# Kernel tuning notes

Measured on AMD Instinct MI355X. Metric: run time of the kernel, lower is better.

The kernel has to match this reference:

```python
import jax, jax.numpy as jnp
import numpy as np

H = 128          # hidden_dim
N = 64           # max_nodes == nodes per graph
G = 512          # num_graphs
E = N * (N - 1) // 2  # policy slots per graph (2016)
LN_EPS = 1e-5


def setup_inputs() -> dict:
    key = jax.random.key(0)
    ks = jax.random.split(key, 8)
    # Complete undirected graph per batch element: canonical edges (i<j), contiguous node blocks.
    iu, ju = np.triu_indices(N, k=1)                      # each [E]
    offs = np.arange(G)[:, None] * N                      # [G,1]
    src = (offs + iu[None, :]).reshape(-1)                # [G*E]
    dst = (offs + ju[None, :]).reshape(-1)
    edge_index = jnp.asarray(np.stack([src, dst]), dtype=jnp.int32)   # [2, G*E]
    num_edges = G * E
    edge_features = jax.random.normal(ks[0], (num_edges, H), dtype=jnp.float32)
    batch = jnp.repeat(jnp.arange(G, dtype=jnp.int32), N)             # [G*N]
    num_nodes_per_graph = jnp.full((G,), N, dtype=jnp.int32)
    s = 0.02
    return {
        "edge_features": edge_features,
        "edge_index": edge_index,
        "batch": batch,
        "num_nodes_per_graph": num_nodes_per_graph,
        "ln_g": jnp.ones((H,), jnp.float32),
        "ln_b": jnp.zeros((H,), jnp.float32),
        "W1": jax.random.normal(ks[1], (H, H), jnp.float32) * s,
        "b1": jnp.zeros((H,), jnp.float32),
        "W2": jax.random.normal(ks[2], (H, H // 2), jnp.float32) * s,
        "b2": jnp.zeros((H // 2,), jnp.float32),
        "W3": jax.random.normal(ks[3], (H // 2, 1), jnp.float32) * s,
        "b3": jnp.zeros((1,), jnp.float32),
    }


def _policy_net(x, ln_g, ln_b, W1, b1, W2, b2, W3, b3):
    mu = jnp.mean(x, axis=-1, keepdims=True)
    var = jnp.mean(jnp.square(x - mu), axis=-1, keepdims=True)
    x = (x - mu) * jax.lax.rsqrt(var + LN_EPS) * ln_g + ln_b
    x = jax.nn.gelu(x @ W1 + b1, approximate=False)   # torch nn.GELU default = exact erf
    x = jax.nn.gelu(x @ W2 + b2, approximate=False)   # (dropout is identity in eval)
    return (x @ W3 + b3)[:, 0]                        # [num_edges]


def reference(edge_features, edge_index, batch, num_nodes_per_graph,
              ln_g, ln_b, W1, b1, W2, b2, W3, b3):
    scores = _policy_net(edge_features, ln_g, ln_b, W1, b1, W2, b2, W3, b3)
    src, dst = edge_index[0], edge_index[1]
    g = src // N                                       # graph id (contiguous node blocks of N)
    ls, ld = src - g * N, dst - g * N                  # local node ids
    i = jnp.minimum(ls, ld)
    j = jnp.maximum(ls, ld)
    # canonical upper-triangular index: i*N - i(i+1)/2 + (j-i-1)
    idx = i * N - i * (i + 1) // 2 + (j - i - 1)
    flat = g * E + idx                                 # [num_edges]
    valid = ls != ld
    logits = jnp.zeros((G * E,), scores.dtype).at[jnp.where(valid, flat, G * E)].set(
        scores, mode="drop")
    return jax.nn.softmax(logits.reshape(G, E), axis=-1)
```

## Files before the change

kernel.cpp:

```cpp
#include <hip/hip_runtime.h>
#include <math.h>

constexpr int Hdim  = 128;
constexpr int Npn   = 64;
constexpr int Eg    = 2016;
constexpr int Gg    = 512;
constexpr int TOT   = Gg * Eg;
constexpr int PITCH = 136;

typedef unsigned short ushortx8 __attribute__((ext_vector_type(8)));
typedef __bf16         bf16x8   __attribute__((ext_vector_type(8)));
typedef float          floatx4  __attribute__((ext_vector_type(4)));

static __device__ __forceinline__ unsigned short f2bf(float f) {
    unsigned int u = __float_as_uint(f);
    u += 0x7FFFu + ((u >> 16) & 1u);
    return (unsigned short)(u >> 16);
}

static __device__ __forceinline__ float gelu_exact(float x) {
    return 0.5f * x * (1.0f + erff(x * 0.70710678118654752440f));
}

static __device__ __forceinline__ floatx4 mfma16(ushortx8 a, ushortx8 b, floatx4 c) {
    return __builtin_amdgcn_mfma_f32_16x16x32_bf16(
        __builtin_bit_cast(bf16x8, a), __builtin_bit_cast(bf16x8, b), c, 0, 0, 0);
}

__global__ __launch_bounds__(256, 3)
void scores_kernel(const float* __restrict__ X, const int* __restrict__ ei,
                   const float* __restrict__ lng, const float* __restrict__ lnb,
                   const float* __restrict__ W1, const float* __restrict__ b1,
                   const float* __restrict__ W2, const float* __restrict__ b2,
                   const float* __restrict__ W3, const float* __restrict__ b3,
                   float* __restrict__ out)
{
    __shared__ unsigned short Xl[64 * PITCH];
    __shared__ unsigned short H1l[64 * PITCH];
    __shared__ float part[4 * 64];

    const int tid  = threadIdx.x;
    const int wave = tid >> 6;
    const int lane = tid & 63;
    const int q    = lane >> 4;
    const int c16  = lane & 15;

    ushortx8 B1f[2][4];
#pragma unroll
    for (int c = 0; c < 2; ++c) {
        const int n = (2 * wave + c) * 16 + c16;
#pragma unroll
        for (int kt = 0; kt < 4; ++kt) {
            ushortx8 f;
#pragma unroll
            for (int j = 0; j < 8; ++j)
                f[j] = f2bf(W1[(kt * 32 + q * 8 + j) * Hdim + n]);
            B1f[c][kt] = f;
        }
    }
    const int n2 = wave * 16 + c16;
    ushortx8 B2f[4];
#pragma unroll
    for (int kt = 0; kt < 4; ++kt) {
        ushortx8 f;
#pragma unroll
        for (int j = 0; j < 8; ++j)
            f[j] = f2bf(W2[(kt * 32 + q * 8 + j) * 64 + n2]);
        B2f[kt] = f;
    }

    const float b1v0 = b1[(2 * wave) * 16 + c16];
    const float b1v1 = b1[(2 * wave + 1) * 16 + c16];
    const float b2v  = b2[n2];
    const float w3v  = W3[n2];
    const float b3v  = b3[0];

    const float4 g4  = ((const float4*)lng)[tid & 31];
    const float4 bb4 = ((const float4*)lnb)[tid & 31];

    for (int t = 0; t < 4; ++t) {
        const int row0 = (blockIdx.x * 4 + t) * 64;

        const float4* Xg = (const float4*)X + (size_t)row0 * 32;
#pragma unroll
        for (int i = 0; i < 8; ++i) {
            float4 v = Xg[tid + 256 * i];
            float s  = v.x + v.y + v.z + v.w;
            float s2 = v.x * v.x + v.y * v.y + v.z * v.z + v.w * v.w;
#pragma unroll
            for (int m = 1; m < 32; m <<= 1) {
                s  += __shfl_xor(s, m);
                s2 += __shfl_xor(s2, m);
            }
            const float mu  = s * 0.0078125f;
            const float var = s2 * 0.0078125f - mu * mu;
            const float rs  = rsqrtf(var + 1e-5f);
            const int row   = (tid + 256 * i) >> 5;
            const float y0 = (v.x - mu) * rs * g4.x + bb4.x;
            const float y1 = (v.y - mu) * rs * g4.y + bb4.y;
            const float y2 = (v.z - mu) * rs * g4.z + bb4.z;
            const float y3 = (v.w - mu) * rs * g4.w + bb4.w;
            uint2 pk;
            pk.x = (unsigned)f2bf(y0) | ((unsigned)f2bf(y1) << 16);
            pk.y = (unsigned)f2bf(y2) | ((unsigned)f2bf(y3) << 16);
            *reinterpret_cast<uint2*>(&Xl[row * PITCH + (tid & 31) * 4]) = pk;
        }
        __syncthreads();

        floatx4 acc[4][2];
#pragma unroll
        for (int rt = 0; rt < 4; ++rt)
#pragma unroll
            for (int c = 0; c < 2; ++c)
                acc[rt][c] = floatx4{0.f, 0.f, 0.f, 0.f};

#pragma unroll
        for (int kt = 0; kt < 4; ++kt) {
            ushortx8 a[4];
#pragma unroll
            for (int rt = 0; rt < 4; ++rt)
                a[rt] = *reinterpret_cast<const ushortx8*>(
                    &Xl[(rt * 16 + c16) * PITCH + kt * 32 + q * 8]);
#pragma unroll
            for (int rt = 0; rt < 4; ++rt) {
                acc[rt][0] = mfma16(a[rt], B1f[0][kt], acc[rt][0]);
                acc[rt][1] = mfma16(a[rt], B1f[1][kt], acc[rt][1]);
            }
        }

#pragma unroll
        for (int rt = 0; rt < 4; ++rt) {
#pragma unroll
            for (int c = 0; c < 2; ++c) {
                const float bb = c ? b1v1 : b1v0;
                const int col  = (2 * wave + c) * 16 + c16;
#pragma unroll
                for (int r = 0; r < 4; ++r) {
                    const float h = gelu_exact(acc[rt][c][r] + bb);
                    H1l[(rt * 16 + q * 4 + r) * PITCH + col] = f2bf(h);
                }
            }
        }
        __syncthreads();

        floatx4 acc2[4];
#pragma unroll
        for (int rt = 0; rt < 4; ++rt) acc2[rt] = floatx4{0.f, 0.f, 0.f, 0.f};
#pragma unroll
        for (int kt = 0; kt < 4; ++kt) {
            ushortx8 a[4];
#pragma unroll
            for (int rt = 0; rt < 4; ++rt)
                a[rt] = *reinterpret_cast<const ushortx8*>(
                    &H1l[(rt * 16 + c16) * PITCH + kt * 32 + q * 8]);
#pragma unroll
            for (int rt = 0; rt < 4; ++rt)
                acc2[rt] = mfma16(a[rt], B2f[kt], acc2[rt]);
        }

#pragma unroll
        for (int rt = 0; rt < 4; ++rt) {
            floatx4 pv;
#pragma unroll
            for (int r = 0; r < 4; ++r)
                pv[r] = gelu_exact(acc2[rt][r] + b2v) * w3v;
#pragma unroll
            for (int m = 1; m < 16; m <<= 1) {
#pragma unroll
                for (int r = 0; r < 4; ++r) pv[r] += __shfl_xor(pv[r], m);
            }
            if (c16 == 0)
                *reinterpret_cast<floatx4*>(&part[wave * 64 + rt * 16 + q * 4]) = pv;
        }
        __syncthreads();

        if (tid < 64) {
            const float sc = b3v + part[tid] + part[64 + tid] + part[128 + tid] + part[192 + tid];
            const int e  = row0 + tid;
            const int s  = ei[e];
            const int d  = ei[TOT + e];
            const int g  = s >> 6;
            const int ls = s & 63, ld = d & 63;
            const int i2 = min(ls, ld), j2 = max(ls, ld);
            if (ls != ld) {
                const int idx = i2 * Npn - ((i2 * (i2 + 1)) >> 1) + (j2 - i2 - 1);
                out[g * Eg + idx] = sc;
            }
        }
        __syncthreads();
    }
}

__global__ __launch_bounds__(256)
void softmax_kernel(float* __restrict__ buf)
{
    __shared__ float red[4];
    const int tid  = threadIdx.x;
    const int wave = tid >> 6;
    const int lane = tid & 63;
    const int base = blockIdx.x * Eg;

    float v[8];
    float mx = -3.4e38f;
#pragma unroll
    for (int k = 0; k < 8; ++k) {
        const int idx = tid + 256 * k;
        v[k] = (idx < Eg) ? buf[base + idx] : -3.4e38f;
        mx = fmaxf(mx, v[k]);
    }
#pragma unroll
    for (int m = 1; m < 64; m <<= 1) mx = fmaxf(mx, __shfl_xor(mx, m));
    if (lane == 0) red[wave] = mx;
    __syncthreads();
    mx = fmaxf(fmaxf(red[0], red[1]), fmaxf(red[2], red[3]));
    __syncthreads();

    float sum = 0.f;
#pragma unroll
    for (int k = 0; k < 8; ++k) {
        const int idx = tid + 256 * k;
        if (idx < Eg) {
            v[k] = expf(v[k] - mx);
            sum += v[k];
        }
    }
#pragma unroll
    for (int m = 1; m < 64; m <<= 1) sum += __shfl_xor(sum, m);
    if (lane == 0) red[wave] = sum;
    __syncthreads();
    sum = red[0] + red[1] + red[2] + red[3];
    const float inv = 1.0f / sum;

#pragma unroll
    for (int k = 0; k < 8; ++k) {
        const int idx = tid + 256 * k;
        if (idx < Eg) buf[base + idx] = v[k] * inv;
    }
}

extern "C" void kernel_launch(void* const* d_in, const int* in_sizes, int n_in,
                              void* d_out, int out_size, void* d_ws, size_t ws_size,
                              hipStream_t stream)
{
    const float* Xf  = (const float*)d_in[0];
    const int*   ei  = (const int*)d_in[1];
    const float* lng = (const float*)d_in[4];
    const float* lnb = (const float*)d_in[5];
    const float* W1  = (const float*)d_in[6];
    const float* b1  = (const float*)d_in[7];
    const float* W2  = (const float*)d_in[8];
    const float* b2  = (const float*)d_in[9];
    const float* W3  = (const float*)d_in[10];
    const float* b3  = (const float*)d_in[11];
    float* out = (float*)d_out;

    hipLaunchKernelGGL(scores_kernel, dim3(TOT / 256), dim3(256), 0, stream,
                       Xf, ei, lng, lnb, W1, b1, W2, b2, W3, b3, out);
    hipLaunchKernelGGL(softmax_kernel, dim3(Gg), dim3(256), 0, stream, out);
}
```

Measured before the change: 786.1 us.

## Prefetch X tiles into LDS asynchronously, fold LayerNorm affine into W1, use fast GELU

```diff
diff --git a/kernel.cpp b/kernel.cpp
--- a/kernel.cpp
+++ b/kernel.cpp
@@ -6,6 +6,9 @@
 constexpr int Eg    = 2016;
 constexpr int Gg    = 512;
 constexpr int TOT   = Gg * Eg;
+constexpr int ROWS  = 32;
+constexpr int TPB   = 16;
+constexpr int NBLK  = TOT / (ROWS * TPB);
 constexpr int PITCH = 136;
 
 typedef unsigned short ushortx8 __attribute__((ext_vector_type(8)));
@@ -18,8 +21,23 @@
     return (unsigned short)(u >> 16);
 }
 
-static __device__ __forceinline__ float gelu_exact(float x) {
-    return 0.5f * x * (1.0f + erff(x * 0.70710678118654752440f));
+static __device__ __forceinline__ unsigned int cvt_pk_bf16(float lo, float hi) {
+    unsigned int r;
+    asm("v_cvt_pk_bf16_f32 %0, %1, %2" : "=v"(r) : "v"(lo), "v"(hi));
+    return r;
+}
+
+static __device__ __forceinline__ float gelu_fast(float x) {
+    const float z = fabsf(x) * 0.70710678118654752440f;
+    const float t = __builtin_amdgcn_rcpf(fmaf(0.3275911f, z, 1.0f));
+    float p = fmaf(1.061405429f, t, -1.453152027f);
+    p = fmaf(p, t,  1.421413741f);
+    p = fmaf(p, t, -0.284496736f);
+    p = fmaf(p, t,  0.254829592f);
+    p *= t;
+    const float e  = __builtin_amdgcn_exp2f(z * z * -1.4426950408889634f);
+    const float er = fmaf(-p, e, 1.0f);
+    return 0.5f * x * (1.0f + copysignf(er, x));
 }
 
 static __device__ __forceinline__ floatx4 mfma16(ushortx8 a, ushortx8 b, floatx4 c) {
@@ -27,7 +45,14 @@
         __builtin_bit_cast(bf16x8, a), __builtin_bit_cast(bf16x8, b), c, 0, 0, 0);
 }
 
-__global__ __launch_bounds__(256, 3)
+typedef __attribute__((address_space(1))) const unsigned int gu32;
+typedef __attribute__((address_space(3))) unsigned int       lu32;
+
+static __device__ __forceinline__ void gload_lds16(const float* g, float* l) {
+    __builtin_amdgcn_global_load_lds((gu32*)(const void*)g, (lu32*)(void*)l, 16, 0, 0);
+}
+
+__global__ __launch_bounds__(256, 4)
 void scores_kernel(const float* __restrict__ X, const int* __restrict__ ei,
                    const float* __restrict__ lng, const float* __restrict__ lnb,
                    const float* __restrict__ W1, const float* __restrict__ b1,
@@ -35,9 +60,10 @@
                    const float* __restrict__ W3, const float* __restrict__ b3,
                    float* __restrict__ out)
 {
-    __shared__ unsigned short Xl[64 * PITCH];
-    __shared__ unsigned short H1l[64 * PITCH];
-    __shared__ float part[4 * 64];
+    __shared__ float          raw[ROWS * Hdim];
+    __shared__ unsigned short Xl [ROWS * PITCH];
+    __shared__ unsigned short H1l[ROWS * PITCH];
+    __shared__ float          part[4 * ROWS];
 
     const int tid  = threadIdx.x;
     const int wave = tid >> 6;
@@ -45,18 +71,37 @@
     const int q    = lane >> 4;
     const int c16  = lane & 15;
 
+    const size_t blockRow0 = (size_t)blockIdx.x * (ROWS * TPB);
+
+    {
+        const float* src = X + blockRow0 * Hdim;
+        const int fo = wave * 256 + lane * 4;
+#pragma unroll
+        for (int k = 0; k < 4; ++k)
+            gload_lds16(src + fo + k * 1024, raw + wave * 256 + k * 1024);
+    }
+
     ushortx8 B1f[2][4];
+    float    b1v[2];
 #pragma unroll
     for (int c = 0; c < 2; ++c) {
         const int n = (2 * wave + c) * 16 + c16;
+        float pb = 0.f;
 #pragma unroll
         for (int kt = 0; kt < 4; ++kt) {
             ushortx8 f;
 #pragma unroll
-            for (int j = 0; j < 8; ++j)
-                f[j] = f2bf(W1[(kt * 32 + q * 8 + j) * Hdim + n]);
+            for (int j = 0; j < 8; ++j) {
+                const int k = kt * 32 + q * 8 + j;
+                const float w = W1[k * Hdim + n];
+                pb   = fmaf(lnb[k], w, pb);
+                f[j] = f2bf(lng[k] * w);
+            }
             B1f[c][kt] = f;
         }
+        pb += __shfl_xor(pb, 16);
+        pb += __shfl_xor(pb, 32);
+        b1v[c] = b1[n] + pb;
     }
     const int n2 = wave * 16 + c16;
     ushortx8 B2f[4];
@@ -68,126 +113,130 @@
             f[j] = f2bf(W2[(kt * 32 + q * 8 + j) * 64 + n2]);
         B2f[kt] = f;
     }
-
-    const float b1v0 = b1[(2 * wave) * 16 + c16];
-    const float b1v1 = b1[(2 * wave + 1) * 16 + c16];
-    const float b2v  = b2[n2];
-    const float w3v  = W3[n2];
-    const float b3v  = b3[0];
-
-    const float4 g4  = ((const float4*)lng)[tid & 31];
-    const float4 bb4 = ((const float4*)lnb)[tid & 31];
-
-    for (int t = 0; t < 4; ++t) {
-        const int row0 = (blockIdx.x * 4 + t) * 64;
-
-        const float4* Xg = (const float4*)X + (size_t)row0 * 32;
-#pragma unroll
-        for (int i = 0; i < 8; ++i) {
-            float4 v = Xg[tid + 256 * i];
-            float s  = v.x + v.y + v.z + v.w;
-            float s2 = v.x * v.x + v.y * v.y + v.z * v.z + v.w * v.w;
-#pragma unroll
-            for (int m = 1; m < 32; m <<= 1) {
-                s  += __shfl_xor(s, m);
-                s2 += __shfl_xor(s2, m);
-            }
-            const float mu  = s * 0.0078125f;
-            const float var = s2 * 0.0078125f - mu * mu;
-            const float rs  = rsqrtf(var + 1e-5f);
-            const int row   = (tid + 256 * i) >> 5;
-            const float y0 = (v.x - mu) * rs * g4.x + bb4.x;
-            const float y1 = (v.y - mu) * rs * g4.y + bb4.y;
-            const float y2 = (v.z - mu) * rs * g4.z + bb4.z;
-            const float y3 = (v.w - mu) * rs * g4.w + bb4.w;
+    const float b2v = b2[n2];
+    const float w3v = W3[n2];
+    const float b3v = b3[0];
+
+    const int row = tid >> 3;
+    const int cg  = tid & 7;
+
+    __syncthreads();
+
+    for (int t = 0; t < TPB; ++t) {
+        float4 x[4];
+#pragma unroll
+        for (int k = 0; k < 4; ++k)
+            x[k] = *reinterpret_cast<const float4*>(&raw[row * Hdim + cg * 4 + k * 32]);
+        float s = 0.f, s2 = 0.f;
+#pragma unroll
+        for (int k = 0; k < 4; ++k) {
+            s += x[k].x + x[k].y + x[k].z + x[k].w;
+            s2 = fmaf(x[k].x, x[k].x, s2);
+            s2 = fmaf(x[k].y, x[k].y, s2);
+            s2 = fmaf(x[k].z, x[k].z, s2);
+            s2 = fmaf(x[k].w, x[k].w, s2);
+        }
+        s  += __shfl_xor(s, 1);  s  += __shfl_xor(s, 2);  s  += __shfl_xor(s, 4);
+        s2 += __shfl_xor(s2, 1); s2 += __shfl_xor(s2, 2); s2 += __shfl_xor(s2, 4);
+        const float mu  = s * 0.0078125f;
+        const float var = fmaf(s2, 0.0078125f, -mu * mu);
+        const float rs  = rsqrtf(var + 1e-5f);
+        const float nm  = -mu * rs;
+#pragma unroll
+        for (int k = 0; k < 4; ++k) {
             uint2 pk;
-            pk.x = (unsigned)f2bf(y0) | ((unsigned)f2bf(y1) << 16);
-            pk.y = (unsigned)f2bf(y2) | ((unsigned)f2bf(y3) << 16);
-            *reinterpret_cast<uint2*>(&Xl[row * PITCH + (tid & 31) * 4]) = pk;
+            pk.x = cvt_pk_bf16(fmaf(x[k].x, rs, nm), fmaf(x[k].y, rs, nm));
+            pk.y = cvt_pk_bf16(fmaf(x[k].z, rs, nm), fmaf(x[k].w, rs, nm));
+            *reinterpret_cast<uint2*>(&Xl[row * PITCH + cg * 4 + k * 32]) = pk;
         }
         __syncthreads();
 
-        floatx4 acc[4][2];
-#pragma unroll
-        for (int rt = 0; rt < 4; ++rt)
+        if (t + 1 < TPB) {
+            const float* src = X + (blockRow0 + (size_t)(t + 1) * ROWS) * Hdim;
+            const int fo = wave * 256 + lane * 4;
+#pragma unroll
+            for (int k = 0; k < 4; ++k)
+                gload_lds16(src + fo + k * 1024, raw + wave * 256 + k * 1024);
+        }
+        int sv = 0, dv = 0;
+        const int e = (int)(blockRow0 + (size_t)t * ROWS) + tid;
+        if (tid < ROWS) { sv = ei[e]; dv = ei[TOT + e]; }
+
+        floatx4 acc[2][2];
+#pragma unroll
+        for (int rt = 0; rt < 2; ++rt)
 #pragma unroll
             for (int c = 0; c < 2; ++c)
                 acc[rt][c] = floatx4{0.f, 0.f, 0.f, 0.f};
-
 #pragma unroll
         for (int kt = 0; kt < 4; ++kt) {
-            ushortx8 a[4];
-#pragma unroll
-            for (int rt = 0; rt < 4; ++rt)
-                a[rt] = *reinterpret_cast<const ushortx8*>(
-                    &Xl[(rt * 16 + c16) * PITCH + kt * 32 + q * 8]);
-#pragma unroll
-            for (int rt = 0; rt < 4; ++rt) {
-                acc[rt][0] = mfma16(a[rt], B1f[0][kt], acc[rt][0]);
-                acc[rt][1] = mfma16(a[rt], B1f[1][kt], acc[rt][1]);
+            ushortx8 a0 = *reinterpret_cast<const ushortx8*>(&Xl[(c16)      * PITCH + kt * 32 + q * 8]);
+            ushortx8 a1 = *reinterpret_cast<const ushortx8*>(&Xl[(16 + c16) * PITCH + kt * 32 + q * 8]);
+            acc[0][0] = mfma16(a0, B1f[0][kt], acc[0][0]);
+            acc[0][1] = mfma16(a0, B1f[1][kt], acc[0][1]);
+            acc[1][0] = mfma16(a1, B1f[0][kt], acc[1][0]);
+            acc[1][1] = mfma16(a1, B1f[1][kt], acc[1][1]);
+        }
+
+#pragma unroll
+        for (int rt = 0; rt < 2; ++rt) {
+#pragma unroll
+            for (int c = 0; c < 2; ++c) {
+                const float bb = b1v[c];
+                const int col  = (2 * wave + c) * 16 + c16;
+                const float h0 = gelu_fast(acc[rt][c][0] + bb);
+                const float h1 = gelu_fast(acc[rt][c][1] + bb);
+                const float h2 = gelu_fast(acc[rt][c][2] + bb);
+                const float h3 = gelu_fast(acc[rt][c][3] + bb);
+                const unsigned int p01 = cvt_pk_bf16(h0, h1);
+                const unsigned int p23 = cvt_pk_bf16(h2, h3);
+                const int rbase = rt * 16 + q * 4;
+                H1l[(rbase + 0) * PITCH + col] = (unsigned short)p01;
+                H1l[(rbase + 1) * PITCH + col] = (unsigned short)(p01 >> 16);
+                H1l[(rbase + 2) * PITCH + col] = (unsigned short)p23;
+                H1l[(rbase + 3) * PITCH + col] = (unsigned short)(p23 >> 16);
             }
         }
-
-#pragma unroll
-        for (int rt = 0; rt < 4; ++rt) {
-#pragma unroll
-            for (int c = 0; c < 2; ++c) {
-                const float bb = c ? b1v1 : b1v0;
-                const int col  = (2 * wave + c) * 16 + c16;
-#pragma unroll
-                for (int r = 0; r < 4; ++r) {
-                    const float h = gelu_exact(acc[rt][c][r] + bb);
-                    H1l[(rt * 16 + q * 4 + r) * PITCH + col] = f2bf(h);
-                }
-            }
-        }
         __syncthreads();
 
-        floatx4 acc2[4];
-#pragma unroll
-        for (int rt = 0; rt < 4; ++rt) acc2[rt] = floatx4{0.f, 0.f, 0.f, 0.f};
+        floatx4 acc2[2];
+        acc2[0] = floatx4{0.f, 0.f, 0.f, 0.f};
+        acc2[1] = floatx4{0.f, 0.f, 0.f, 0.f};
 #pragma unroll
         for (int kt = 0; kt < 4; ++kt) {
-            ushortx8 a[4];
-#pragma unroll
-            for (int rt = 0; rt < 4; ++rt)
-                a[rt] = *reinterpret_cast<const ushortx8*>(
-                    &H1l[(rt * 16 + c16) * PITCH + kt * 32 + q * 8]);
-#pragma unroll
-            for (int rt = 0; rt < 4; ++rt)
-                acc2[rt] = mfma16(a[rt], B2f[kt], acc2[rt]);
-        }
-
-#pragma unroll
-        for (int rt = 0; rt < 4; ++rt) {
+            ushortx8 a0 = *reinterpret_cast<const ushortx8*>(&H1l[(c16)      * PITCH + kt * 32 + q * 8]);
+            ushortx8 a1 = *reinterpret_cast<const ushortx8*>(&H1l[(16 + c16) * PITCH + kt * 32 + q * 8]);
+            acc2[0] = mfma16(a0, B2f[kt], acc2[0]);
+            acc2[1] = mfma16(a1, B2f[kt], acc2[1]);
+        }
+
+#pragma unroll
+        for (int rt = 0; rt < 2; ++rt) {
             floatx4 pv;
 #pragma unroll
             for (int r = 0; r < 4; ++r)
-                pv[r] = gelu_exact(acc2[rt][r] + b2v) * w3v;
+                pv[r] = gelu_fast(acc2[rt][r] + b2v) * w3v;
 #pragma unroll
             for (int m = 1; m < 16; m <<= 1) {
 #pragma unroll
                 for (int r = 0; r < 4; ++r) pv[r] += __shfl_xor(pv[r], m);
             }
             if (c16 == 0)
-                *reinterpret_cast<floatx4*>(&part[wave * 64 + rt * 16 + q * 4]) = pv;
+                *reinterpret_cast<floatx4*>(&part[wave * ROWS + rt * 16 + q * 4]) = pv;
         }
         __syncthreads();
 
-        if (tid < 64) {
-            const float sc = b3v + part[tid] + part[64 + tid] + part[128 + tid] + part[192 + tid];
-            const int e  = row0 + tid;
-            const int s  = ei[e];
-            const int d  = ei[TOT + e];
-            const int g  = s >> 6;
-            const int ls = s & 63, ld = d & 63;
+        if (tid < ROWS) {
+            const float sc = b3v + part[tid] + part[ROWS + tid]
+                           + part[2 * ROWS + tid] + part[3 * ROWS + tid];
+            const int g  = sv >> 6;
+            const int ls = sv & 63, ld = dv & 63;
             const int i2 = min(ls, ld), j2 = max(ls, ld);
             if (ls != ld) {
                 const int idx = i2 * Npn - ((i2 * (i2 + 1)) >> 1) + (j2 - i2 - 1);
                 out[g * Eg + idx] = sc;
             }
         }
-        __syncthreads();
     }
 }
 
@@ -220,7 +269,7 @@
     for (int k = 0; k < 8; ++k) {
         const int idx = tid + 256 * k;
         if (idx < Eg) {
-            v[k] = expf(v[k] - mx);
+            v[k] = __builtin_amdgcn_exp2f((v[k] - mx) * 1.4426950408889634f);
             sum += v[k];
         }
     }
@@ -254,7 +303,7 @@
     const float* b3  = (const float*)d_in[11];
     float* out = (float*)d_out;
 
-    hipLaunchKernelGGL(scores_kernel, dim3(TOT / 256), dim3(256), 0, stream,
+    hipLaunchKernelGGL(scores_kernel, dim3(NBLK), dim3(256), 0, stream,
                        Xf, ei, lng, lnb, W1, b1, W2, b2, W3, b3, out);
     hipLaunchKernelGGL(softmax_kernel, dim3(Gg), dim3(256), 0, stream, out);
 }
```

After: 760.8 us. 3.2% less time.
